# Performance work log

Measured on AMD Instinct MI355X. Metric: run time of the kernel, lower is better.

Reference implementation:

```python
import jax, jax.numpy as jnp
import numpy as np

N_WAY = 2
K_SHOT = 5
C = 320
NPTS = 2048
NQ = 2
K_PROTO = 100  # hardcoded k=100 in forward
N_CLS = N_WAY + 1
SIGMA = 1.0
NEG = -1e9


def _l2norm(x, eps=1e-8):
    return x / (jnp.linalg.norm(x, axis=-1, keepdims=True) + eps)


def _class_prototypes(feat, mask, k):
    """Multi-prototype masked pooling for one class.
    feat: [M, C] point features; mask: [M] float (1 = belongs to class).
    Picks k masked seed points, assigns every masked point to its
    nearest (cosine) seed, and returns the k masked cluster means.
    """
    M = feat.shape[0]
    # deterministic seeds: first k masked points (tie-break by index)
    score = mask - jnp.arange(M, dtype=feat.dtype) * 1e-9
    _, seed_idx = jax.lax.top_k(score, k)
    seeds = feat[seed_idx]                      # [k, C]
    sim = _l2norm(feat) @ _l2norm(seeds).T      # [M, k]
    assign = jnp.argmax(sim, axis=1)            # [M]
    onehot = jax.nn.one_hot(assign, k, dtype=feat.dtype) * mask[:, None]  # [M, k]
    num = onehot.T @ feat                       # [k, C]
    den = onehot.sum(axis=0)[:, None] + 1e-8
    return num / den


def _fg_prototypes(support_feat, fg_mask, k):
    # support_feat [n_way, k_shot, C, N] -> per-class point sets [n_way, k_shot*N, C]
    feat = support_feat.transpose(0, 1, 3, 2).reshape(N_WAY, -1, C)
    m = fg_mask.reshape(N_WAY, -1).astype(feat.dtype)
    protos = jax.vmap(lambda f, mm: _class_prototypes(f, mm, k))(feat, m)  # [n_way, k, C]
    labels = jnp.repeat(jnp.arange(1, N_WAY + 1), k)                        # classes 1..n_way
    return protos.reshape(-1, C), jax.nn.one_hot(labels, N_CLS, dtype=feat.dtype)


def _bg_prototypes(support_feat, bg_mask, k):
    feat = support_feat.transpose(0, 1, 3, 2).reshape(-1, C)   # all shots pooled
    m = bg_mask.reshape(-1).astype(feat.dtype)
    protos = _class_prototypes(feat, m, k)                      # [k, C]
    labels = jnp.zeros((k,), dtype=jnp.int32)                   # class 0 = background
    return protos, jax.nn.one_hot(labels, N_CLS, dtype=feat.dtype)


def _predict(prototypes, proto_onehot, qfeat, qlabels):
    # cosine similarity [M, P], per-class max over that class's prototypes
    sim = (_l2norm(qfeat) @ _l2norm(prototypes).T) / SIGMA        # [M, P]
    cls_mask = proto_onehot.T[None] > 0                            # [1, ncls, P]
    pred = jnp.max(jnp.where(cls_mask, sim[:, None, :], NEG), axis=-1)  # [M, ncls]
    logp = jax.nn.log_softmax(pred, axis=-1)
    loss = -jnp.mean(jnp.take_along_axis(logp, qlabels.reshape(-1, 1), axis=1))
    query_pred = pred.reshape(NQ, NPTS, N_CLS).transpose(0, 2, 1)  # [NQ, ncls, NPTS]
    return loss, query_pred


def reference(support_feat, query_feat, support_y, query_y):
    fg_mask = support_y
    bg_mask = 1 - support_y
    fg_protos, fg_labels = _fg_prototypes(support_feat, fg_mask, K_PROTO)
    bg_protos, bg_labels = _bg_prototypes(support_feat, bg_mask, K_PROTO)
    prototypes = jnp.concatenate([bg_protos, fg_protos], axis=0)           # [P, C]
    proto_labels = jnp.concatenate([bg_labels, fg_labels], axis=0)         # [P, ncls]

    qfeat = query_feat.transpose(0, 2, 1).reshape(-1, C)                   # [NQ*NPTS, C]
    loss, query_pred = _predict(prototypes, proto_labels, qfeat, query_y)
    # the forward adds computeCrossEntropyLoss(query_pred, query_y): same CE again
    loss = loss * 2.0

    # post-hoc per-point confidence thresholding (vectorized Python loop)
    qp = jnp.concatenate([query_pred[0], query_pred[1]], axis=-1)          # [ncls, NQ*NPTS]
    predictions = jnp.argmax(qp, axis=0)
    confidences = jnp.max(qp, axis=0)
    final = jnp.where(confidences > jnp.mean(confidences), predictions, -1)
    final_labels = jnp.stack([final[:NPTS], final[NPTS:]], axis=0)         # [2, NPTS]
    return loss, query_pred, final_labels


def setup_inputs() -> dict:
    key = jax.random.key(0)
    k1, k2, k3, k4 = jax.random.split(key, 4)
    return {
        "support_feat": jax.random.normal(k1, (N_WAY, K_SHOT, C, NPTS), dtype=jnp.float32),
        "query_feat": jax.random.normal(k2, (NQ, C, NPTS), dtype=jnp.float32),
        "support_y": jax.random.randint(k3, (N_WAY, K_SHOT, NPTS), 0, 2, dtype=jnp.int32),
        "query_y": jax.random.randint(k4, (NQ, NPTS), 0, 3, dtype=jnp.int32),
    }
```

## Files before the change

kernel.cpp:

```cpp
#include <hip/hip_runtime.h>
#include <math.h>

#define C 320
#define NPTS 2048
#define SUPPTS 20480
#define QPTS 4096
#define KP 100
#define NCLS 3
#define PSTRIDE 300

__global__ __launch_bounds__(64) void k_protoseed(const float* __restrict__ sup,
                                                  const int* __restrict__ sy,
                                                  float* __restrict__ pbufT) {
    int p    = blockIdx.x;
    int lane = threadIdx.x;
    int prob = (p < 100) ? 2 : ((p < 200) ? 0 : 1);
    int rank = (p < 100) ? p : ((p < 200) ? p - 100 : p - 200);
    int M    = (prob == 2) ? SUPPTS : 10240;
    int base = (prob == 1) ? 10240 : 0;
    int found = 0, sp = 0;
    for (int chunk = 0; chunk < M; chunk += 64) {
        int yy = sy[base + chunk + lane];
        int m  = (prob == 2) ? (1 - yy) : yy;
        unsigned long long bal = __ballot(m != 0);
        int cnt = __popcll(bal);
        if (found + cnt > rank) {
            int need = rank - found;
            int prefix = __popcll(bal & ((1ull << lane) - 1ull));
            unsigned long long match = __ballot(m && (prefix == need));
            int pos = __ffsll((unsigned long long)match) - 1;
            sp = base + chunk + pos;
            break;
        }
        found += cnt;
    }
    const float* fb = sup + ((size_t)(sp >> 11) * C) * NPTS + (sp & 2047);
    float v[5]; float s = 0.f;
    #pragma unroll
    for (int i = 0; i < 5; i++) {
        v[i] = fb[(size_t)(lane + i * 64) * NPTS];
        s += v[i] * v[i];
    }
    #pragma unroll
    for (int off = 32; off > 0; off >>= 1) s += __shfl_down(s, off);
    s = __shfl(s, 0);
    float r = 1.0f / (sqrtf(s) + 1e-8f);
    #pragma unroll
    for (int i = 0; i < 5; i++)
        pbufT[(size_t)(lane + i * 64) * PSTRIDE + p] = v[i] * r;
}

__global__ __launch_bounds__(128) void k_assign(const float* __restrict__ sup,
                                                const float* __restrict__ pbT,
                                                float* __restrict__ pmaxv,
                                                int* __restrict__ pmaxj) {
    __shared__ float shp[C * 20];
    int b = blockIdx.x, jt = blockIdx.y, tid = threadIdx.x;
    int prob, pt, gbase, aoff;
    if (b < 40)       { prob = 0; pt = b * 256;         gbase = 0;     aoff = 0; }
    else if (b < 80)  { prob = 1; pt = (b - 40) * 256;  gbase = 10240; aoff = 10240; }
    else              { prob = 2; pt = (b - 80) * 256;  gbase = 0;     aoff = 20480; }
    int j0 = jt * 20;
    int col0 = (prob == 2) ? 0 : (100 + prob * 100);
    for (int i = tid; i < C * 20; i += 128) {
        int j = i % 20, c = i / 20;
        shp[i] = pbT[(size_t)c * PSTRIDE + col0 + j0 + j];
    }
    __syncthreads();
    int g = gbase + pt + tid * 2;
    const float* fb = sup + ((size_t)(g >> 11) * C) * NPTS + (g & 2047);
    float acc0[20], acc1[20];
    #pragma unroll
    for (int j = 0; j < 20; j++) { acc0[j] = 0.f; acc1[j] = 0.f; }
    float2 pf[8];
    #pragma unroll
    for (int k = 0; k < 8; k++) pf[k] = *(const float2*)(fb + (size_t)k * NPTS);
    for (int cc = 0; cc < C; cc += 8) {
        float2 cur[8];
        #pragma unroll
        for (int k = 0; k < 8; k++) cur[k] = pf[k];
        if (cc + 8 < C) {
            #pragma unroll
            for (int k = 0; k < 8; k++) pf[k] = *(const float2*)(fb + (size_t)(cc + 8 + k) * NPTS);
        }
        #pragma unroll
        for (int k = 0; k < 8; k++) {
            const float4* r = (const float4*)&shp[(cc + k) * 20];
            float4 a = r[0], d1 = r[1], d2 = r[2], d3 = r[3], d4 = r[4];
            float px = cur[k].x, py = cur[k].y;
            acc0[0]+=px*a.x;  acc1[0]+=py*a.x;  acc0[1]+=px*a.y;  acc1[1]+=py*a.y;
            acc0[2]+=px*a.z;  acc1[2]+=py*a.z;  acc0[3]+=px*a.w;  acc1[3]+=py*a.w;
            acc0[4]+=px*d1.x; acc1[4]+=py*d1.x; acc0[5]+=px*d1.y; acc1[5]+=py*d1.y;
            acc0[6]+=px*d1.z; acc1[6]+=py*d1.z; acc0[7]+=px*d1.w; acc1[7]+=py*d1.w;
            acc0[8]+=px*d2.x; acc1[8]+=py*d2.x; acc0[9]+=px*d2.y; acc1[9]+=py*d2.y;
            acc0[10]+=px*d2.z;acc1[10]+=py*d2.z;acc0[11]+=px*d2.w;acc1[11]+=py*d2.w;
            acc0[12]+=px*d3.x;acc1[12]+=py*d3.x;acc0[13]+=px*d3.y;acc1[13]+=py*d3.y;
            acc0[14]+=px*d3.z;acc1[14]+=py*d3.z;acc0[15]+=px*d3.w;acc1[15]+=py*d3.w;
            acc0[16]+=px*d4.x;acc1[16]+=py*d4.x;acc0[17]+=px*d4.y;acc1[17]+=py*d4.y;
            acc0[18]+=px*d4.z;acc1[18]+=py*d4.z;acc0[19]+=px*d4.w;acc1[19]+=py*d4.w;
        }
    }
    float bv0 = acc0[0]; int bj0 = 0;
    float bv1 = acc1[0]; int bj1 = 0;
    #pragma unroll
    for (int j = 1; j < 20; j++) {
        if (acc0[j] > bv0) { bv0 = acc0[j]; bj0 = j; }
        if (acc1[j] > bv1) { bv1 = acc1[j]; bj1 = j; }
    }
    size_t a0 = (size_t)jt * 40960 + (aoff + pt + tid * 2);
    pmaxv[a0]     = bv0; pmaxj[a0]     = j0 + bj0;
    pmaxv[a0 + 1] = bv1; pmaxj[a0 + 1] = j0 + bj1;
}

__global__ __launch_bounds__(256) void k_combine_dst(const float* __restrict__ pmaxv,
                                                     const int* __restrict__ pmaxj,
                                                     const int* __restrict__ sy,
                                                     int* __restrict__ dst,
                                                     float* __restrict__ loss) {
    int g = blockIdx.x * 256 + threadIdx.x;
    if (g == 0) loss[0] = 0.f;
    if (g == 1) loss[1] = 0.f;
    float bvf = pmaxv[g]; int bjf = pmaxj[g];
    #pragma unroll
    for (int t = 1; t < 5; t++) {
        float v = pmaxv[(size_t)t * 40960 + g];
        if (v > bvf) { bvf = v; bjf = pmaxj[(size_t)t * 40960 + g]; }
    }
    float bvb = pmaxv[SUPPTS + g]; int bjb = pmaxj[SUPPTS + g];
    #pragma unroll
    for (int t = 1; t < 5; t++) {
        float v = pmaxv[(size_t)t * 40960 + SUPPTS + g];
        if (v > bvb) { bvb = v; bjb = pmaxj[(size_t)t * 40960 + SUPPTS + g]; }
    }
    int way = (g >= 10240) ? 1 : 0;
    dst[g] = sy[g] ? (100 + way * 100 + bjf) : bjb;
}

__global__ __launch_bounds__(256) void k_accum_lds(const float* __restrict__ sup,
                                                   const int* __restrict__ dst,
                                                   float* __restrict__ part,
                                                   float* __restrict__ cnt) {
    __shared__ float bins[8 * 800];
    __shared__ float scnt[800];
    int bx = blockIdx.x;
    int ct = blockIdx.y;
    int tid = threadIdx.x;
    int copy = tid & 3;
    int ws = bx >> 1, half = bx & 1;
    int w = (ws >= 5) ? 1 : 0;
    int nbase = half * 1024;
    for (int i = tid; i < 8 * 800; i += 256) bins[i] = 0.f;
    if (ct == 0) { for (int i = tid; i < 800; i += 256) scnt[i] = 0.f; }
    int dreg[4];
    #pragma unroll
    for (int sub = 0; sub < 4; sub++) {
        int d = dst[ws * 2048 + nbase + sub * 256 + tid];
        dreg[sub] = (d < 100) ? d : (d - w * 100);
    }
    __syncthreads();
    if (ct == 0) {
        #pragma unroll
        for (int sub = 0; sub < 4; sub++) atomicAdd(&scnt[copy * 200 + dreg[sub]], 1.0f);
    }
    const float* base = sup + ((size_t)ws * C + ct * 8) * NPTS + nbase;
    for (int cl = 0; cl < 8; cl++) {
        const float* row = base + (size_t)cl * NPTS;
        #pragma unroll
        for (int sub = 0; sub < 4; sub++)
            atomicAdd(&bins[cl * 800 + copy * 200 + dreg[sub]], row[sub * 256 + tid]);
    }
    __syncthreads();
    float* pout = part + (size_t)(bx * 40 + ct) * 1600;
    for (int i = tid; i < 8 * 200; i += 256) {
        int bin = i >> 3, cl = i & 7;
        float s = bins[cl * 800 + bin] + bins[cl * 800 + 200 + bin]
                + bins[cl * 800 + 400 + bin] + bins[cl * 800 + 600 + bin];
        pout[i] = s;
    }
    if (ct == 0 && tid < 200)
        cnt[bx * 200 + tid] = scnt[tid] + scnt[200 + tid] + scnt[400 + tid] + scnt[600 + tid];
}

__global__ __launch_bounds__(64) void k_reduce_proto(const float* __restrict__ part,
                                                     const float* __restrict__ cnt,
                                                     float* __restrict__ phatT) {
    int d   = blockIdx.x;
    int tid = threadIdx.x;
    int local, s0, ns;
    if (d < 100)      { local = d;       s0 = 0;  ns = 20; }
    else if (d < 200) { local = d;       s0 = 0;  ns = 10; }
    else              { local = d - 100; s0 = 10; ns = 10; }
    float dn = 0.f;
    for (int k = 0; k < ns; k++) dn += cnt[(s0 + k) * 200 + local];
    float inv = 1.0f / (dn + 1e-8f);
    float vals[5]; float sq = 0.f;
    #pragma unroll
    for (int i = 0; i < 5; i++) {
        int c = tid + i * 64;
        int ct = c >> 3, cl = c & 7;
        float s = 0.f;
        for (int k = 0; k < ns; k++)
            s += part[(size_t)((s0 + k) * 40 + ct) * 1600 + local * 8 + cl];
        float v = s * inv;
        vals[i] = v; sq += v * v;
    }
    #pragma unroll
    for (int off = 32; off > 0; off >>= 1) sq += __shfl_down(sq, off);
    sq = __shfl(sq, 0);
    float rn = 1.0f / (sqrtf(sq) + 1e-8f);
    #pragma unroll
    for (int i = 0; i < 5; i++)
        phatT[(size_t)(tid + i * 64) * PSTRIDE + d] = vals[i] * rn;
}

__global__ __launch_bounds__(256) void k_qpartial(const float* __restrict__ qry,
                                                  const float* __restrict__ phT,
                                                  float* __restrict__ qmaxv,
                                                  float* __restrict__ qrn) {
    __shared__ float shp[C * 16];
    __shared__ float red[3 * 64 * 45];
    int pb = blockIdx.x, jt = blockIdx.y, tid = threadIdx.x;
    int wave = tid >> 6, lane = tid & 63;
    int j0 = jt * 10;
    for (int i = tid; i < C * 10; i += 256) {
        int j = i % 10, c = i / 10;
        shp[c * 16 + j] = phT[(size_t)c * PSTRIDE + j0 + j];
    }
    __syncthreads();
    int m = pb * 256 + lane * 4;
    int c0 = wave * 80;
    const float* fb = qry + ((size_t)(m >> 11) * C + c0) * NPTS + (m & 2047);
    float acc[4][10];
    #pragma unroll
    for (int p = 0; p < 4; p++)
        #pragma unroll
        for (int j = 0; j < 10; j++) acc[p][j] = 0.f;
    float qn[4] = {0.f, 0.f, 0.f, 0.f};
    float4 pf[8];
    #pragma unroll
    for (int k = 0; k < 8; k++) pf[k] = *(const float4*)(fb + (size_t)k * NPTS);
    for (int cc = 0; cc < 80; cc += 8) {
        float4 cur[8];
        #pragma unroll
        for (int k = 0; k < 8; k++) cur[k] = pf[k];
        if (cc + 8 < 80) {
            #pragma unroll
            for (int k = 0; k < 8; k++) pf[k] = *(const float4*)(fb + (size_t)(cc + 8 + k) * NPTS);
        }
        #pragma unroll
        for (int k = 0; k < 8; k++) {
            const float* row = &shp[(c0 + cc + k) * 16];
            float4 p0 = ((const float4*)row)[0];
            float4 p1 = ((const float4*)row)[1];
            float2 p2 = ((const float2*)row)[4];
            float pr[10] = {p0.x,p0.y,p0.z,p0.w,p1.x,p1.y,p1.z,p1.w,p2.x,p2.y};
            float4 cv = cur[k];
            if (jt == 0) {
                qn[0] += cv.x*cv.x; qn[1] += cv.y*cv.y; qn[2] += cv.z*cv.z; qn[3] += cv.w*cv.w;
            }
            #pragma unroll
            for (int j = 0; j < 10; j++) {
                acc[0][j] += cv.x * pr[j];
                acc[1][j] += cv.y * pr[j];
                acc[2][j] += cv.z * pr[j];
                acc[3][j] += cv.w * pr[j];
            }
        }
    }
    if (wave > 0) {
        float* my = red + ((wave - 1) * 64 + lane) * 45;
        #pragma unroll
        for (int p = 0; p < 4; p++)
            #pragma unroll
            for (int j = 0; j < 10; j++) my[p * 10 + j] = acc[p][j];
        #pragma unroll
        for (int p = 0; p < 4; p++) my[40 + p] = qn[p];
    }
    __syncthreads();
    if (wave == 0) {
        #pragma unroll
        for (int w = 0; w < 3; w++) {
            const float* my = red + (w * 64 + lane) * 45;
            #pragma unroll
            for (int p = 0; p < 4; p++)
                #pragma unroll
                for (int j = 0; j < 10; j++) acc[p][j] += my[p * 10 + j];
            #pragma unroll
            for (int p = 0; p < 4; p++) qn[p] += my[40 + p];
        }
        #pragma unroll
        for (int p = 0; p < 4; p++) {
            float bv = acc[p][0];
            #pragma unroll
            for (int j = 1; j < 10; j++) bv = fmaxf(bv, acc[p][j]);
            qmaxv[(size_t)(m + p) * 30 + jt] = bv;
        }
        if (jt == 0) {
            #pragma unroll
            for (int p = 0; p < 4; p++) qrn[m + p] = 1.0f / (sqrtf(qn[p]) + 1e-8f);
        }
    }
}

__global__ __launch_bounds__(256) void k_pred(const float* __restrict__ qmaxv,
                                              const float* __restrict__ qrn,
                                              const int* __restrict__ qy,
                                              float* __restrict__ out,
                                              float* __restrict__ lossacc,
                                              float* __restrict__ cbuf,
                                              int* __restrict__ lbuf) {
    __shared__ float redL[256];
    __shared__ float redC[256];
    int tid = threadIdx.x;
    int m = blockIdx.x * 256 + tid;
    float rn = qrn[m];
    float pred[NCLS];
    #pragma unroll
    for (int cls = 0; cls < NCLS; cls++) {
        float g = qmaxv[(size_t)m * 30 + cls * 10];
        #pragma unroll
        for (int t = 1; t < 10; t++) g = fmaxf(g, qmaxv[(size_t)m * 30 + cls * 10 + t]);
        pred[cls] = rn * g;
    }
    int q = m >> 11, n = m & 2047;
    #pragma unroll
    for (int cls = 0; cls < NCLS; cls++)
        out[1 + ((size_t)(q * NCLS + cls)) * NPTS + n] = pred[cls];
    float mx = fmaxf(pred[0], fmaxf(pred[1], pred[2]));
    float lse = mx + logf(expf(pred[0] - mx) + expf(pred[1] - mx) + expf(pred[2] - mx));
    int lab = 0; float cf = pred[0];
    if (pred[1] > cf) { cf = pred[1]; lab = 1; }
    if (pred[2] > cf) { cf = pred[2]; lab = 2; }
    cbuf[m] = cf; lbuf[m] = lab;
    redL[tid] = lse - pred[qy[m]];
    redC[tid] = cf;
    __syncthreads();
    for (int off = 128; off > 0; off >>= 1) {
        if (tid < off) { redL[tid] += redL[tid + off]; redC[tid] += redC[tid + off]; }
        __syncthreads();
    }
    if (tid == 0) {
        atomicAdd(&lossacc[0], redL[0]);
        atomicAdd(&lossacc[1], redC[0]);
    }
}

__global__ __launch_bounds__(256) void k_final(const float* __restrict__ cbuf,
                                               const int* __restrict__ lbuf,
                                               const float* __restrict__ lossacc,
                                               float* __restrict__ out) {
    int m = blockIdx.x * 256 + threadIdx.x;
    float mean = lossacc[1] / (float)QPTS;
    float cf = cbuf[m];
    out[1 + 2 * NCLS * NPTS + m] = (cf > mean) ? (float)lbuf[m] : -1.0f;
    if (m == 0) out[0] = 2.0f * lossacc[0] / (float)QPTS;
}

extern "C" void kernel_launch(void* const* d_in, const int* in_sizes, int n_in,
                              void* d_out, int out_size, void* d_ws, size_t ws_size,
                              hipStream_t stream) {
    const float* sup = (const float*)d_in[0];
    const float* qry = (const float*)d_in[1];
    const int*   sy  = (const int*)d_in[2];
    const int*   qy  = (const int*)d_in[3];
    float* out = (float*)d_out;

    float* f      = (float*)d_ws;
    float* qrn    = f;
    float* cnt    = qrn + QPTS;
    float* pbufT  = cnt + 4000;
    float* phatT  = pbufT + 96000;
    float* loss   = phatT + 96000;
    int*   dstb   = (int*)(loss + 4);
    float* trans  = (float*)(dstb + SUPPTS);
    float* pmaxv  = trans;
    int*   pmaxj  = (int*)(pmaxv + 204800);
    float* part   = trans;
    float* qmaxv  = trans;
    float* cbuf   = qmaxv + 122880;
    int*   lbuf   = (int*)(cbuf + QPTS);

    k_protoseed<<<300, 64, 0, stream>>>(sup, sy, pbufT);
    {
        dim3 grid(160, 5);
        k_assign<<<grid, 128, 0, stream>>>(sup, pbufT, pmaxv, pmaxj);
    }
    k_combine_dst<<<80, 256, 0, stream>>>(pmaxv, pmaxj, sy, dstb, loss);
    {
        dim3 grid(20, 40);
        k_accum_lds<<<grid, 256, 0, stream>>>(sup, dstb, part, cnt);
    }
    k_reduce_proto<<<300, 64, 0, stream>>>(part, cnt, phatT);
    {
        dim3 grid(16, 30);
        k_qpartial<<<grid, 256, 0, stream>>>(qry, phatT, qmaxv, qrn);
    }
    k_pred<<<16, 256, 0, stream>>>(qmaxv, qrn, qy, out, loss, cbuf, lbuf);
    k_final<<<16, 256, 0, stream>>>(cbuf, lbuf, loss, out);
}
```

Measured before the change: 240.3 us.

## Compute only the relevant class assignment per support point using its label

```diff
diff --git a/kernel.cpp b/kernel.cpp
--- a/kernel.cpp
+++ b/kernel.cpp
@@ -50,66 +50,61 @@
         pbufT[(size_t)(lane + i * 64) * PSTRIDE + p] = v[i] * r;
 }
 
-__global__ __launch_bounds__(128) void k_assign(const float* __restrict__ sup,
+__global__ __launch_bounds__(256) void k_assign(const float* __restrict__ sup,
+                                                const int* __restrict__ sy,
                                                 const float* __restrict__ pbT,
                                                 float* __restrict__ pmaxv,
                                                 int* __restrict__ pmaxj) {
-    __shared__ float shp[C * 20];
+    __shared__ float shp[2 * C * 12];
     int b = blockIdx.x, jt = blockIdx.y, tid = threadIdx.x;
-    int prob, pt, gbase, aoff;
-    if (b < 40)       { prob = 0; pt = b * 256;         gbase = 0;     aoff = 0; }
-    else if (b < 80)  { prob = 1; pt = (b - 40) * 256;  gbase = 10240; aoff = 10240; }
-    else              { prob = 2; pt = (b - 80) * 256;  gbase = 0;     aoff = 20480; }
-    int j0 = jt * 20;
-    int col0 = (prob == 2) ? 0 : (100 + prob * 100);
-    for (int i = tid; i < C * 20; i += 128) {
-        int j = i % 20, c = i / 20;
-        shp[i] = pbT[(size_t)c * PSTRIDE + col0 + j0 + j];
-    }
-    __syncthreads();
-    int g = gbase + pt + tid * 2;
+    int w = (b >= 40) ? 1 : 0;
+    int colf = 100 + w * 100 + jt * 10;
+    int colb = jt * 10;
+    for (int i = tid; i < C * 10; i += 256) {
+        int c = i / 10, j = i % 10;
+        shp[c * 12 + j]          = pbT[(size_t)c * PSTRIDE + colf + j];
+        shp[C * 12 + c * 12 + j] = pbT[(size_t)c * PSTRIDE + colb + j];
+    }
+    int g = b * 256 + tid;
+    int sel = sy[g] ? 0 : (C * 12);
+    __syncthreads();
     const float* fb = sup + ((size_t)(g >> 11) * C) * NPTS + (g & 2047);
-    float acc0[20], acc1[20];
-    #pragma unroll
-    for (int j = 0; j < 20; j++) { acc0[j] = 0.f; acc1[j] = 0.f; }
-    float2 pf[8];
-    #pragma unroll
-    for (int k = 0; k < 8; k++) pf[k] = *(const float2*)(fb + (size_t)k * NPTS);
+    float acc[10];
+    #pragma unroll
+    for (int j = 0; j < 10; j++) acc[j] = 0.f;
+    float pf[8];
+    #pragma unroll
+    for (int k = 0; k < 8; k++) pf[k] = fb[(size_t)k * NPTS];
     for (int cc = 0; cc < C; cc += 8) {
-        float2 cur[8];
+        float cur[8];
         #pragma unroll
         for (int k = 0; k < 8; k++) cur[k] = pf[k];
         if (cc + 8 < C) {
             #pragma unroll
-            for (int k = 0; k < 8; k++) pf[k] = *(const float2*)(fb + (size_t)(cc + 8 + k) * NPTS);
+            for (int k = 0; k < 8; k++) pf[k] = fb[(size_t)(cc + 8 + k) * NPTS];
         }
         #pragma unroll
         for (int k = 0; k < 8; k++) {
-            const float4* r = (const float4*)&shp[(cc + k) * 20];
-            float4 a = r[0], d1 = r[1], d2 = r[2], d3 = r[3], d4 = r[4];
-            float px = cur[k].x, py = cur[k].y;
-            acc0[0]+=px*a.x;  acc1[0]+=py*a.x;  acc0[1]+=px*a.y;  acc1[1]+=py*a.y;
-            acc0[2]+=px*a.z;  acc1[2]+=py*a.z;  acc0[3]+=px*a.w;  acc1[3]+=py*a.w;
-            acc0[4]+=px*d1.x; acc1[4]+=py*d1.x; acc0[5]+=px*d1.y; acc1[5]+=py*d1.y;
-            acc0[6]+=px*d1.z; acc1[6]+=py*d1.z; acc0[7]+=px*d1.w; acc1[7]+=py*d1.w;
-            acc0[8]+=px*d2.x; acc1[8]+=py*d2.x; acc0[9]+=px*d2.y; acc1[9]+=py*d2.y;
-            acc0[10]+=px*d2.z;acc1[10]+=py*d2.z;acc0[11]+=px*d2.w;acc1[11]+=py*d2.w;
-            acc0[12]+=px*d3.x;acc1[12]+=py*d3.x;acc0[13]+=px*d3.y;acc1[13]+=py*d3.y;
-            acc0[14]+=px*d3.z;acc1[14]+=py*d3.z;acc0[15]+=px*d3.w;acc1[15]+=py*d3.w;
-            acc0[16]+=px*d4.x;acc1[16]+=py*d4.x;acc0[17]+=px*d4.y;acc1[17]+=py*d4.y;
-            acc0[18]+=px*d4.z;acc1[18]+=py*d4.z;acc0[19]+=px*d4.w;acc1[19]+=py*d4.w;
-        }
-    }
-    float bv0 = acc0[0]; int bj0 = 0;
-    float bv1 = acc1[0]; int bj1 = 0;
-    #pragma unroll
-    for (int j = 1; j < 20; j++) {
-        if (acc0[j] > bv0) { bv0 = acc0[j]; bj0 = j; }
-        if (acc1[j] > bv1) { bv1 = acc1[j]; bj1 = j; }
-    }
-    size_t a0 = (size_t)jt * 40960 + (aoff + pt + tid * 2);
-    pmaxv[a0]     = bv0; pmaxj[a0]     = j0 + bj0;
-    pmaxv[a0 + 1] = bv1; pmaxj[a0 + 1] = j0 + bj1;
+            const float* row = &shp[sel + (cc + k) * 12];
+            float4 p0 = ((const float4*)row)[0];
+            float4 p1 = ((const float4*)row)[1];
+            float2 p2 = *(const float2*)(row + 8);
+            float px = cur[k];
+            acc[0] += px * p0.x; acc[1] += px * p0.y;
+            acc[2] += px * p0.z; acc[3] += px * p0.w;
+            acc[4] += px * p1.x; acc[5] += px * p1.y;
+            acc[6] += px * p1.z; acc[7] += px * p1.w;
+            acc[8] += px * p2.x; acc[9] += px * p2.y;
+        }
+    }
+    float bv = acc[0]; int bj = 0;
+    #pragma unroll
+    for (int j = 1; j < 10; j++) {
+        if (acc[j] > bv) { bv = acc[j]; bj = j; }
+    }
+    size_t a0 = (size_t)jt * 20480 + g;
+    pmaxv[a0] = bv;
+    pmaxj[a0] = jt * 10 + bj;
 }
 
 __global__ __launch_bounds__(256) void k_combine_dst(const float* __restrict__ pmaxv,
@@ -120,20 +115,14 @@
     int g = blockIdx.x * 256 + threadIdx.x;
     if (g == 0) loss[0] = 0.f;
     if (g == 1) loss[1] = 0.f;
-    float bvf = pmaxv[g]; int bjf = pmaxj[g];
-    #pragma unroll
-    for (int t = 1; t < 5; t++) {
-        float v = pmaxv[(size_t)t * 40960 + g];
-        if (v > bvf) { bvf = v; bjf = pmaxj[(size_t)t * 40960 + g]; }
-    }
-    float bvb = pmaxv[SUPPTS + g]; int bjb = pmaxj[SUPPTS + g];
-    #pragma unroll
-    for (int t = 1; t < 5; t++) {
-        float v = pmaxv[(size_t)t * 40960 + SUPPTS + g];
-        if (v > bvb) { bvb = v; bjb = pmaxj[(size_t)t * 40960 + SUPPTS + g]; }
+    float bv = pmaxv[g]; int bj = pmaxj[g];
+    #pragma unroll
+    for (int t = 1; t < 10; t++) {
+        float v = pmaxv[(size_t)t * 20480 + g];
+        if (v > bv) { bv = v; bj = pmaxj[(size_t)t * 20480 + g]; }
     }
     int way = (g >= 10240) ? 1 : 0;
-    dst[g] = sy[g] ? (100 + way * 100 + bjf) : bjb;
+    dst[g] = sy[g] ? (100 + way * 100 + bj) : bj;
 }
 
 __global__ __launch_bounds__(256) void k_accum_lds(const float* __restrict__ sup,
@@ -382,8 +371,8 @@
 
     k_protoseed<<<300, 64, 0, stream>>>(sup, sy, pbufT);
     {
-        dim3 grid(160, 5);
-        k_assign<<<grid, 128, 0, stream>>>(sup, pbufT, pmaxv, pmaxj);
+        dim3 grid(80, 10);
+        k_assign<<<grid, 256, 0, stream>>>(sup, sy, pbufT, pmaxv, pmaxj);
     }
     k_combine_dst<<<80, 256, 0, stream>>>(pmaxv, pmaxj, sy, dstb, loss);
     {
```

New measurement: 246.5 us. +2.6%, slower.
